# Performance work log

Hardware: AMD Instinct MI355X
Metric: run time of the kernel (lower is better)

The kernel has to match this reference:

```python
import jax, jax.numpy as jnp
import numpy as np

N, L, C_IN, DEM = 64, 2048, 256, 10


def setup_inputs() -> dict:
    key = jax.random.key(0)
    k1, k2, k3, k4 = jax.random.split(key, 4)
    timesteps = jax.random.normal(k1, (N, L, C_IN), dtype=jnp.float32)
    dem = jax.random.normal(k2, (N, DEM), dtype=jnp.float32)
    W1 = jax.random.normal(k3, (DEM, 40), dtype=jnp.float32) * 0.1
    b1 = jnp.zeros((40,), dtype=jnp.float32)
    W2 = jax.random.normal(k4, (40, 20), dtype=jnp.float32) * 0.1
    b2 = jnp.zeros((20,), dtype=jnp.float32)
    return {"timesteps": timesteps, "dem": dem, "W1": W1, "b1": b1, "W2": W2, "b2": b2}


def reference(timesteps, dem, W1, b1, W2, b2):
    # dem MLP: Linear(10,40) -> ReLU -> (Dropout p=0, eval) -> Linear(40,20) -> ReLU
    h = jax.nn.relu(dem @ W1 + b1)
    dem_emb = jax.nn.relu(h @ W2 + b2)                     # (N, 20)
    n, l, _ = timesteps.shape
    dem_b = jnp.broadcast_to(dem_emb[:, None, :], (n, l, dem_emb.shape[-1]))
    x = jnp.concatenate([timesteps, dem_b], axis=-1)       # (N, L, C)
    # Causal nonzero-average pool: avg_pool1d with kernel=L over (L-1)-left-padded
    # sequence == at step t, sum(x[:t+1]) / count_nonzero(x[:t+1]) per channel.
    csum = jnp.cumsum(x, axis=1)                           # (N, L, C)
    ccnt = jnp.cumsum((x != 0).astype(x.dtype), axis=1)    # (N, L, C)
    p_avg = csum / jnp.maximum(ccnt, 1.0)
    return jax.nn.relu(p_avg)
```

## Files before the change

### kernel.cpp

```cpp
#include <hip/hip_runtime.h>


#define NB 64
#define LL 2048
#define CIN 256
#define COUT 276
#define DEMD 10
#define H1 40
#define H2 20

#define SEGS 64
#define SROWS (LL / SEGS)
#define UB 8
#define NBATCH (SROWS / UB)
#define NUNITS (NB * SEGS)
#define NBLK (NUNITS / 4)

__global__ __launch_bounds__(256) void pme_part(
    const float* __restrict__ ts,
    float* __restrict__ part)
{
    const int tid  = threadIdx.x;
    const int w    = tid >> 6;
    const int lane = tid & 63;

    const int unit = blockIdx.x * 4 + w;
    const int seg  = unit & (SEGS - 1);
    const int n    = unit >> 6;

    const float4* tp = (const float4*)(ts + ((size_t)n * LL + seg * SROWS) * CIN) + lane;

    float4 sum = make_float4(0.f, 0.f, 0.f, 0.f);
    float4 ctv = make_float4(0.f, 0.f, 0.f, 0.f);

    float4 v[2][UB];
#pragma unroll
    for (int u = 0; u < UB; ++u)
        v[0][u] = tp[(size_t)u * (CIN / 4)];

    for (int bb = 0; bb < NBATCH; ++bb) {
        const int cur = bb & 1;
        if (bb + 1 < NBATCH) {
#pragma unroll
            for (int u = 0; u < UB; ++u)
                v[cur ^ 1][u] = tp[(size_t)((bb + 1) * UB + u) * (CIN / 4)];
        }
#pragma unroll
        for (int u = 0; u < UB; ++u) {
            float4 x = v[cur][u];
            sum.x += x.x; ctv.x += (x.x != 0.f) ? 1.f : 0.f;
            sum.y += x.y; ctv.y += (x.y != 0.f) ? 1.f : 0.f;
            sum.z += x.z; ctv.z += (x.z != 0.f) ? 1.f : 0.f;
            sum.w += x.w; ctv.w += (x.w != 0.f) ? 1.f : 0.f;
        }
    }

    float4* pp = (float4*)part + ((size_t)n * SEGS + seg) * 128 + lane * 2;
    pp[0] = make_float4(sum.x, ctv.x, sum.y, ctv.y);
    pp[1] = make_float4(sum.z, ctv.z, sum.w, ctv.w);
}

__global__ __launch_bounds__(256) void pme_scan(
    const float* __restrict__ ts,
    const float* __restrict__ part,
    const float* __restrict__ dem,
    const float* __restrict__ W1, const float* __restrict__ b1,
    const float* __restrict__ W2, const float* __restrict__ b2,
    float* __restrict__ out)
{
    __shared__ float4 QS[4][64];
    __shared__ float4 QC[4][64];

    const int tid  = threadIdx.x;
    const int w    = tid >> 6;
    const int lane = tid & 63;

    const int b       = blockIdx.x;
    const int n       = b >> 4;
    const int grp     = b & 15;
    const int segbase = grp * 4;
    const int seg     = segbase + w;
    const int q       = grp;

    const float4* base = (const float4*)part + (size_t)n * SEGS * 128 + lane * 2;

    float4 A = make_float4(0.f, 0.f, 0.f, 0.f);
    float4 B = make_float4(0.f, 0.f, 0.f, 0.f);
    for (int s = w * q; s < w * q + q; ++s) {
        float4 a = base[(size_t)s * 128];
        float4 c = base[(size_t)s * 128 + 1];
        A.x += a.x; A.y += a.y; A.z += a.z; A.w += a.w;
        B.x += c.x; B.y += c.y; B.z += c.z; B.w += c.w;
    }
    QS[w][lane] = A;
    QC[w][lane] = B;
    __syncthreads();

    A = make_float4(0.f, 0.f, 0.f, 0.f);
    B = make_float4(0.f, 0.f, 0.f, 0.f);
#pragma unroll
    for (int s = 0; s < 4; ++s) {
        float4 a = QS[s][lane];
        float4 c = QC[s][lane];
        A.x += a.x; A.y += a.y; A.z += a.z; A.w += a.w;
        B.x += c.x; B.y += c.y; B.z += c.z; B.w += c.w;
    }
    for (int s = segbase; s < seg; ++s) {
        float4 a = base[(size_t)s * 128];
        float4 c = base[(size_t)s * 128 + 1];
        A.x += a.x; A.y += a.y; A.z += a.z; A.w += a.w;
        B.x += c.x; B.y += c.y; B.z += c.z; B.w += c.w;
    }
    float4 acc = make_float4(A.x, A.z, B.x, B.z);
    float4 cnt = make_float4(A.y, A.w, B.y, B.w);

    const int tr = lane / 5;
    const int tj = lane - tr * 5;
    float4 e4q;
    {
        const float* dn = dem + n * DEMD;
        float d[DEMD];
#pragma unroll
        for (int i = 0; i < DEMD; ++i)
            d[i] = dn[i];
        float e0 = b2[tj * 4 + 0], e1 = b2[tj * 4 + 1], e2 = b2[tj * 4 + 2], e3 = b2[tj * 4 + 3];
#pragma unroll
        for (int k = 0; k < H1; ++k) {
            float hk = b1[k];
#pragma unroll
            for (int i = 0; i < DEMD; ++i)
                hk += d[i] * W1[i * H1 + k];
            hk = fmaxf(hk, 0.f);
            e0 += hk * W2[k * H2 + tj * 4 + 0];
            e1 += hk * W2[k * H2 + tj * 4 + 1];
            e2 += hk * W2[k * H2 + tj * 4 + 2];
            e3 += hk * W2[k * H2 + tj * 4 + 3];
        }
        e4q = make_float4(fmaxf(e0, 0.f), fmaxf(e1, 0.f), fmaxf(e2, 0.f), fmaxf(e3, 0.f));
    }

    const float4* tp = (const float4*)(ts + ((size_t)n * LL + seg * SROWS) * CIN) + lane;
    float* oprow = out + ((size_t)n * LL + seg * SROWS) * COUT;

    float4 v[2][UB];
#pragma unroll
    for (int u = 0; u < UB; ++u)
        v[0][u] = tp[(size_t)u * (CIN / 4)];

    for (int bb = 0; bb < NBATCH; ++bb) {
        const int cur = bb & 1;
        if (bb + 1 < NBATCH) {
#pragma unroll
            for (int u = 0; u < UB; ++u)
                v[cur ^ 1][u] = tp[(size_t)((bb + 1) * UB + u) * (CIN / 4)];
        }
#pragma unroll
        for (int u = 0; u < UB; ++u) {
            float4 x = v[cur][u];
            float4 r;
            acc.x += x.x; cnt.x += (x.x != 0.f) ? 1.f : 0.f;
            acc.y += x.y; cnt.y += (x.y != 0.f) ? 1.f : 0.f;
            acc.z += x.z; cnt.z += (x.z != 0.f) ? 1.f : 0.f;
            acc.w += x.w; cnt.w += (x.w != 0.f) ? 1.f : 0.f;
            r.x = fmaxf(acc.x * __builtin_amdgcn_rcpf(fmaxf(cnt.x, 1.f)), 0.f);
            r.y = fmaxf(acc.y * __builtin_amdgcn_rcpf(fmaxf(cnt.y, 1.f)), 0.f);
            r.z = fmaxf(acc.z * __builtin_amdgcn_rcpf(fmaxf(cnt.z, 1.f)), 0.f);
            r.w = fmaxf(acc.w * __builtin_amdgcn_rcpf(fmaxf(cnt.w, 1.f)), 0.f);
            *(float4*)(oprow + (size_t)(bb * UB + u) * COUT + lane * 4) = r;
        }
    }

    float* tailbase = oprow + CIN;
    if (lane < 60) {
        *(float4*)(tailbase + (size_t)(0  + tr) * COUT + tj * 4) = e4q;
        *(float4*)(tailbase + (size_t)(12 + tr) * COUT + tj * 4) = e4q;
    }
    if (lane < 40)
        *(float4*)(tailbase + (size_t)(24 + tr) * COUT + tj * 4) = e4q;
}

extern "C" void kernel_launch(void* const* d_in, const int* in_sizes, int n_in,
                              void* d_out, int out_size, void* d_ws, size_t ws_size,
                              hipStream_t stream) {
    const float* ts  = (const float*)d_in[0];
    const float* dem = (const float*)d_in[1];
    const float* W1  = (const float*)d_in[2];
    const float* b1  = (const float*)d_in[3];
    const float* W2  = (const float*)d_in[4];
    const float* b2  = (const float*)d_in[5];
    float* out  = (float*)d_out;
    float* part = (float*)d_ws;

    pme_part<<<NBLK, 256, 0, stream>>>(ts, part);
    pme_scan<<<NBLK, 256, 0, stream>>>(ts, part, dem, W1, b1, W2, b2, out);
}
```

Measured before the change: 300.6 us.

## Compute intra-block prefix in part kernel and prefetch inputs before carry loads

The partial-sum kernel now does an in-block inclusive prefix across its 4 segments through shared memory, so the scan kernel only reads one partial per earlier 4-segment group plus one neighbour, instead of summing many per-segment partials. The first batch of timestep loads is issued before the carry reads, so that global load overlaps the carry computation and the dem MLP. This adds a barrier and some shared memory traffic to the part kernel, and keeps more registers live earlier in the scan kernel.

```diff
diff --git a/kernel.cpp b/kernel.cpp
--- a/kernel.cpp
+++ b/kernel.cpp
@@ -20,6 +20,9 @@
     const float* __restrict__ ts,
     float* __restrict__ part)
 {
+    __shared__ float4 P0[4][64];
+    __shared__ float4 P1[4][64];
+
     const int tid  = threadIdx.x;
     const int w    = tid >> 6;
     const int lane = tid & 63;
@@ -55,9 +58,21 @@
         }
     }
 
+    P0[w][lane] = make_float4(sum.x, ctv.x, sum.y, ctv.y);
+    P1[w][lane] = make_float4(sum.z, ctv.z, sum.w, ctv.w);
+    __syncthreads();
+
+    float4 A = make_float4(0.f, 0.f, 0.f, 0.f);
+    float4 C = make_float4(0.f, 0.f, 0.f, 0.f);
+    for (int e = 0; e <= w; ++e) {
+        float4 a = P0[e][lane];
+        float4 c = P1[e][lane];
+        A.x += a.x; A.y += a.y; A.z += a.z; A.w += a.w;
+        C.x += c.x; C.y += c.y; C.z += c.z; C.w += c.w;
+    }
     float4* pp = (float4*)part + ((size_t)n * SEGS + seg) * 128 + lane * 2;
-    pp[0] = make_float4(sum.x, ctv.x, sum.y, ctv.y);
-    pp[1] = make_float4(sum.z, ctv.z, sum.w, ctv.w);
+    pp[0] = A;
+    pp[1] = C;
 }
 
 __global__ __launch_bounds__(256) void pme_scan(
@@ -80,39 +95,45 @@
     const int grp     = b & 15;
     const int segbase = grp * 4;
     const int seg     = segbase + w;
-    const int q       = grp;
+
+    const float4* tp = (const float4*)(ts + ((size_t)n * LL + seg * SROWS) * CIN) + lane;
+
+    float4 v[2][UB];
+#pragma unroll
+    for (int u = 0; u < UB; ++u)
+        v[0][u] = tp[(size_t)u * (CIN / 4)];
 
     const float4* base = (const float4*)part + (size_t)n * SEGS * 128 + lane * 2;
 
     float4 A = make_float4(0.f, 0.f, 0.f, 0.f);
-    float4 B = make_float4(0.f, 0.f, 0.f, 0.f);
-    for (int s = w * q; s < w * q + q; ++s) {
-        float4 a = base[(size_t)s * 128];
-        float4 c = base[(size_t)s * 128 + 1];
-        A.x += a.x; A.y += a.y; A.z += a.z; A.w += a.w;
-        B.x += c.x; B.y += c.y; B.z += c.z; B.w += c.w;
+    float4 C = make_float4(0.f, 0.f, 0.f, 0.f);
+    for (int g = w; g < grp; g += 4) {
+        float4 a = base[(size_t)(4 * g + 3) * 128];
+        float4 c = base[(size_t)(4 * g + 3) * 128 + 1];
+        A.x += a.x; A.y += a.y; A.z += a.z; A.w += a.w;
+        C.x += c.x; C.y += c.y; C.z += c.z; C.w += c.w;
     }
     QS[w][lane] = A;
-    QC[w][lane] = B;
+    QC[w][lane] = C;
     __syncthreads();
 
     A = make_float4(0.f, 0.f, 0.f, 0.f);
-    B = make_float4(0.f, 0.f, 0.f, 0.f);
+    C = make_float4(0.f, 0.f, 0.f, 0.f);
 #pragma unroll
     for (int s = 0; s < 4; ++s) {
         float4 a = QS[s][lane];
         float4 c = QC[s][lane];
         A.x += a.x; A.y += a.y; A.z += a.z; A.w += a.w;
-        B.x += c.x; B.y += c.y; B.z += c.z; B.w += c.w;
-    }
-    for (int s = segbase; s < seg; ++s) {
-        float4 a = base[(size_t)s * 128];
-        float4 c = base[(size_t)s * 128 + 1];
-        A.x += a.x; A.y += a.y; A.z += a.z; A.w += a.w;
-        B.x += c.x; B.y += c.y; B.z += c.z; B.w += c.w;
-    }
-    float4 acc = make_float4(A.x, A.z, B.x, B.z);
-    float4 cnt = make_float4(A.y, A.w, B.y, B.w);
+        C.x += c.x; C.y += c.y; C.z += c.z; C.w += c.w;
+    }
+    if (w > 0) {
+        float4 a = base[(size_t)(segbase + w - 1) * 128];
+        float4 c = base[(size_t)(segbase + w - 1) * 128 + 1];
+        A.x += a.x; A.y += a.y; A.z += a.z; A.w += a.w;
+        C.x += c.x; C.y += c.y; C.z += c.z; C.w += c.w;
+    }
+    float4 acc = make_float4(A.x, A.z, C.x, C.z);
+    float4 cnt = make_float4(A.y, A.w, C.y, C.w);
 
     const int tr = lane / 5;
     const int tj = lane - tr * 5;
@@ -139,13 +160,7 @@
         e4q = make_float4(fmaxf(e0, 0.f), fmaxf(e1, 0.f), fmaxf(e2, 0.f), fmaxf(e3, 0.f));
     }
 
-    const float4* tp = (const float4*)(ts + ((size_t)n * LL + seg * SROWS) * CIN) + lane;
     float* oprow = out + ((size_t)n * LL + seg * SROWS) * COUT;
-
-    float4 v[2][UB];
-#pragma unroll
-    for (int u = 0; u < UB; ++u)
-        v[0][u] = tp[(size_t)u * (CIN / 4)];
 
     for (int bb = 0; bb < NBATCH; ++bb) {
         const int cur = bb & 1;
```

New measurement: 300.9 us. No clear change (+0.1%).
